# Performance work log

Hardware: AMD Instinct MI355X
Metric: run time of the kernel (lower is better)

## Reference

```python
import jax, jax.numpy as jnp
import numpy as np
from jax import lax

B, T, D_IN, D_PROJ, D_OUT, LORDER = 16, 2048, 1024, 512, 1024, 20


def setup_inputs() -> dict:
    key = jax.random.key(0)
    k1, k2, k3, k4 = jax.random.split(key, 4)
    s = 0.05
    return {
        "input": jax.random.normal(k1, (B, T, D_IN), dtype=jnp.float32),
        "in_cache": jnp.zeros((B, D_PROJ, LORDER - 1), dtype=jnp.float32),
        "W_lin": jax.random.normal(k2, (D_IN, D_PROJ), dtype=jnp.float32) * s,
        "conv_w": jax.random.normal(k3, (D_PROJ, LORDER), dtype=jnp.float32) * s,
        "W_aff": jax.random.normal(k4, (D_PROJ, D_OUT), dtype=jnp.float32) * s,
        "b_aff": jnp.zeros((D_OUT,), dtype=jnp.float32),
    }


def reference(input, in_cache, W_lin, conv_w, W_aff, b_aff):
    L = conv_w.shape[1]
    # 1) linear down-projection (no bias): [B,T,Din] -> [B,T,Dp]
    x = jnp.einsum("btd,dp->btp", input, W_lin)
    # 2) FSMN causal depthwise memory block with streaming cache
    xt = jnp.swapaxes(x, 1, 2)                       # [B,Dp,T]
    cat = jnp.concatenate([in_cache, xt], axis=2)    # [B,Dp,T+L-1]
    out_cache = cat[:, :, -(L - 1):]                 # last L-1 frames for next chunk
    # depthwise conv over time, VALID padding -> output length T
    y = lax.conv_general_dilated(
        cat, conv_w[:, None, :],                      # rhs [Dp,1,L]
        window_strides=(1,), padding="VALID",
        dimension_numbers=("NCH", "OIH", "NCH"),
        feature_group_count=conv_w.shape[0])
    m = jnp.swapaxes(y + xt, 1, 2)                   # residual add, back to [B,T,Dp]
    # 3) affine up-projection + 4) ReLU
    out = jax.nn.relu(jnp.einsum("btp,po->bto", m, W_aff) + b_aff)
    return (out, out_cache)
```

## Files before the change

### kernel.cpp

```cpp
#include <hip/hip_runtime.h>
#include <cstdint>
#include <cstddef>

#define B_  16
#define T_  2048
#define DIN 1024
#define DPJ 512
#define DOUT 1024
#define LORD 20
#define HALO (LORD - 1)
#define M_ROWS (B_ * T_)
#define OUT0_ELEMS ((size_t)M_ROWS * DOUT)
#define CACHE_ELEMS ((size_t)B_ * DPJ * (LORD - 1))

typedef __bf16 bf16_t;
typedef __bf16 bf16x2 __attribute__((ext_vector_type(2)));
typedef __bf16 bf16x4 __attribute__((ext_vector_type(4)));
typedef __bf16 bf16x8 __attribute__((ext_vector_type(8)));
typedef float  f32x4  __attribute__((ext_vector_type(4)));

__device__ __forceinline__ void async_load16(const bf16_t* g, bf16_t* lds_base) {
    __builtin_amdgcn_global_load_lds(
        (const __attribute__((address_space(1))) unsigned int*)g,
        (__attribute__((address_space(3))) unsigned int*)lds_base,
        16, 0, 0);
}

__global__ __launch_bounds__(256) void prep_weights(
    const float* __restrict__ Wl, const float* __restrict__ Wa,
    bf16_t* __restrict__ WlT, bf16_t* __restrict__ WaT) {
    int idx = blockIdx.x * 256 + threadIdx.x;
    const int n1 = DIN * DPJ;
    if (idx < n1) {
        int k = idx / DPJ, n = idx - k * DPJ;
        WlT[(size_t)n * DIN + k] = (bf16_t)Wl[idx];
    } else {
        int j = idx - n1;
        if (j < DPJ * DOUT) {
            int k = j / DOUT, n = j - k * DOUT;
            WaT[(size_t)n * DPJ + k] = (bf16_t)Wa[j];
        }
    }
}

__global__ __launch_bounds__(256) void gemm_f32a(
    const float* __restrict__ A, const bf16_t* __restrict__ Bt,
    bf16_t* __restrict__ C, const int M, const int N, const int K) {
    __shared__ bf16_t sA[128 * 64];
    __shared__ bf16_t sB[128 * 64];

    const int tid  = threadIdx.x;
    const int lane = tid & 63;
    const int wave = tid >> 6;
    const int row0 = blockIdx.x * 128;
    const int col0 = blockIdx.y * 128;

    const int lr   = lane >> 3;
    const int jsw  = (lane & 7) ^ lr;
    const bf16_t* gB0 = Bt + (size_t)(col0 + wave * 32 + lr) * K + jsw * 8;
    bf16_t* lB0 = sB + wave * 2048;

    const int ar  = tid >> 4;
    const int ac4 = tid & 15;
    const float* gA0 = A + (size_t)(row0 + ar) * K + ac4 * 4;
    const int aj = ac4 >> 1, ah = ac4 & 1;
    const int asw = ((aj ^ (ar & 7)) << 3) + ah * 4;

    const int wm = (wave >> 1) * 64;
    const int wn = (wave & 1) * 64;
    const int fr = lane & 15;
    const int fk = lane >> 4;

    const f32x4 zero = {0.f, 0.f, 0.f, 0.f};
    f32x4 acc[4][4];
#pragma unroll
    for (int mt = 0; mt < 4; ++mt)
#pragma unroll
        for (int nt = 0; nt < 4; ++nt) acc[mt][nt] = zero;

    for (int k0 = 0; k0 < K; k0 += 64) {
        __syncthreads();
        float4 av[8];
#pragma unroll
        for (int i = 0; i < 8; ++i)
            av[i] = *(const float4*)(gA0 + (size_t)i * 16 * K + k0);
#pragma unroll
        for (int c = 0; c < 4; ++c)
            async_load16(gB0 + (size_t)c * 8 * K + k0, lB0 + c * 512);
#pragma unroll
        for (int i = 0; i < 8; ++i) {
            bf16x4 o = { (bf16_t)av[i].x, (bf16_t)av[i].y,
                         (bf16_t)av[i].z, (bf16_t)av[i].w };
            *(bf16x4*)(sA + (i * 16 + ar) * 64 + asw) = o;
        }
        __syncthreads();

#pragma unroll
        for (int h = 0; h < 2; ++h) {
            bf16x8 af[4], bfr[4];
#pragma unroll
            for (int mt = 0; mt < 4; ++mt) {
                int r = wm + mt * 16 + fr;
                int j = h * 4 + fk;
                af[mt] = *(const bf16x8*)(sA + r * 64 + ((j ^ (r & 7)) << 3));
            }
#pragma unroll
            for (int nt = 0; nt < 4; ++nt) {
                int r = wn + nt * 16 + fr;
                int j = h * 4 + fk;
                bfr[nt] = *(const bf16x8*)(sB + r * 64 + ((j ^ (r & 7)) << 3));
            }
#pragma unroll
            for (int mt = 0; mt < 4; ++mt)
#pragma unroll
                for (int nt = 0; nt < 4; ++nt)
                    acc[mt][nt] = __builtin_amdgcn_mfma_f32_16x16x32_bf16(
                        af[mt], bfr[nt], acc[mt][nt], 0, 0, 0);
        }
    }

    const int er = row0 + wm + (lane >> 4) * 4;
    const int ec = col0 + wn + (lane & 15);
#pragma unroll
    for (int mt = 0; mt < 4; ++mt)
#pragma unroll
        for (int nt = 0; nt < 4; ++nt)
#pragma unroll
            for (int rr = 0; rr < 4; ++rr)
                C[(size_t)(er + mt * 16 + rr) * N + (ec + nt * 16)] =
                    (bf16_t)acc[mt][nt][rr];
}

__global__ __launch_bounds__(256) void gemm_bt_relu(
    const bf16_t* __restrict__ A, const bf16_t* __restrict__ Bt,
    float* __restrict__ C, const float* __restrict__ bias,
    const int M, const int N, const int K) {
    __shared__ bf16_t sA[128 * 64];
    __shared__ bf16_t sB[128 * 64];

    const int tid  = threadIdx.x;
    const int lane = tid & 63;
    const int wave = tid >> 6;
    const int row0 = blockIdx.x * 128;
    const int col0 = blockIdx.y * 128;

    const int lr   = lane >> 3;
    const int jsw  = (lane & 7) ^ lr;
    const bf16_t* gA0 = A  + (size_t)(row0 + wave * 32 + lr) * K + jsw * 8;
    const bf16_t* gB0 = Bt + (size_t)(col0 + wave * 32 + lr) * K + jsw * 8;
    bf16_t* lA0 = sA + wave * 2048;
    bf16_t* lB0 = sB + wave * 2048;

    const int wm = (wave >> 1) * 64;
    const int wn = (wave & 1) * 64;
    const int fr = lane & 15;
    const int fk = lane >> 4;

    const f32x4 zero = {0.f, 0.f, 0.f, 0.f};
    f32x4 acc[4][4];
#pragma unroll
    for (int mt = 0; mt < 4; ++mt)
#pragma unroll
        for (int nt = 0; nt < 4; ++nt) acc[mt][nt] = zero;

    for (int k0 = 0; k0 < K; k0 += 64) {
        __syncthreads();
#pragma unroll
        for (int c = 0; c < 4; ++c) {
            async_load16(gA0 + (size_t)c * 8 * K + k0, lA0 + c * 512);
            async_load16(gB0 + (size_t)c * 8 * K + k0, lB0 + c * 512);
        }
        __syncthreads();

#pragma unroll
        for (int h = 0; h < 2; ++h) {
            bf16x8 af[4], bfr[4];
#pragma unroll
            for (int mt = 0; mt < 4; ++mt) {
                int r = wm + mt * 16 + fr;
                int j = h * 4 + fk;
                af[mt] = *(const bf16x8*)(sA + r * 64 + ((j ^ (r & 7)) << 3));
            }
#pragma unroll
            for (int nt = 0; nt < 4; ++nt) {
                int r = wn + nt * 16 + fr;
                int j = h * 4 + fk;
                bfr[nt] = *(const bf16x8*)(sB + r * 64 + ((j ^ (r & 7)) << 3));
            }
#pragma unroll
            for (int mt = 0; mt < 4; ++mt)
#pragma unroll
                for (int nt = 0; nt < 4; ++nt)
                    acc[mt][nt] = __builtin_amdgcn_mfma_f32_16x16x32_bf16(
                        af[mt], bfr[nt], acc[mt][nt], 0, 0, 0);
        }
    }

    const int er = row0 + wm + (lane >> 4) * 4;
    const int ec = col0 + wn + (lane & 15);
#pragma unroll
    for (int nt = 0; nt < 4; ++nt) {
        float bb = bias[ec + nt * 16];
#pragma unroll
        for (int mt = 0; mt < 4; ++mt)
#pragma unroll
            for (int rr = 0; rr < 4; ++rr) {
                float v = acc[mt][nt][rr] + bb;
                C[(size_t)(er + mt * 16 + rr) * N + (ec + nt * 16)] =
                    v > 0.f ? v : 0.f;
            }
    }
}

#define TT 64
#define PPT 128
__global__ __launch_bounds__(256) void dwconv_tiled(
    const bf16_t* __restrict__ x, const float* __restrict__ cache,
    const float* __restrict__ cw, bf16_t* __restrict__ m) {
    __shared__ float sx[(TT + HALO) * PPT];

    const int tid = threadIdx.x;
    const int t0  = blockIdx.x * TT;
    const int b   = blockIdx.y;
    const int p0  = blockIdx.z * PPT;

    for (int c = tid; c < (TT + HALO) * PPT / 8; c += 256) {
        int r    = c >> 4;
        int col  = (c & 15) << 3;
        int trow = t0 - HALO + r;
        float* dst = sx + r * PPT + col;
        if (trow >= 0) {
            bf16x8 v = *(const bf16x8*)(x + ((size_t)(b * T_ + trow)) * DPJ + p0 + col);
#pragma unroll
            for (int i = 0; i < 8; ++i) dst[i] = (float)v[i];
        } else {
#pragma unroll
            for (int i = 0; i < 8; ++i)
                dst[i] = cache[((size_t)b * DPJ + p0 + col + i) * HALO + (trow + HALO)];
        }
    }
    __syncthreads();

    const int pp   = tid & 63;
    const int half = tid >> 6;
    const int tb   = half * 16;
    const float2* sx2 = (const float2*)sx;

    const int pg = p0 + 2 * pp;
    float2 w[LORD];
#pragma unroll
    for (int l = 0; l < LORD; ++l) {
        w[l].x = cw[pg * LORD + l];
        w[l].y = cw[(pg + 1) * LORD + l];
    }

    float2 win[LORD];
#pragma unroll
    for (int i = 0; i < HALO; ++i) win[i] = sx2[(tb + i) * 64 + pp];

#pragma unroll
    for (int tl = 0; tl < 16; ++tl) {
        float2 nv = sx2[(tb + tl + HALO) * 64 + pp];
        win[(tl + HALO) % LORD] = nv;
        float2 s = nv;
#pragma unroll
        for (int l = 0; l < LORD; ++l) {
            float2 v = win[(tl + l) % LORD];
            s.x += w[l].x * v.x;
            s.y += w[l].y * v.y;
        }
        bf16x2 o = { (bf16_t)s.x, (bf16_t)s.y };
        *(bf16x2*)(m + ((size_t)(b * T_ + t0 + tb + tl)) * DPJ + pg) = o;
    }
}

__global__ __launch_bounds__(256) void cache_out(
    const bf16_t* __restrict__ x, float* __restrict__ oc) {
    int idx = blockIdx.x * 256 + threadIdx.x;
    if (idx < (int)CACHE_ELEMS) {
        int b = idx / (DPJ * (LORD - 1));
        int rem = idx % (DPJ * (LORD - 1));
        int p = rem / (LORD - 1);
        int j = rem % (LORD - 1);
        oc[idx] = (float)x[((size_t)(b * T_ + T_ - (LORD - 1) + j)) * DPJ + p];
    }
}

extern "C" void kernel_launch(void* const* d_in, const int* in_sizes, int n_in,
                              void* d_out, int out_size, void* d_ws, size_t ws_size,
                              hipStream_t stream) {
    const float* input    = (const float*)d_in[0];
    const float* in_cache = (const float*)d_in[1];
    const float* W_lin    = (const float*)d_in[2];
    const float* conv_w   = (const float*)d_in[3];
    const float* W_aff    = (const float*)d_in[4];
    const float* b_aff    = (const float*)d_in[5];
    float* out = (float*)d_out;

    char* ws = (char*)d_ws;
    bf16_t* x_buf = (bf16_t*)(ws);
    bf16_t* m_buf = (bf16_t*)(ws + 33554432);
    bf16_t* WlinT = (bf16_t*)(ws + 67108864);
    bf16_t* WaffT = (bf16_t*)(ws + 67108864 + 1048576);

    prep_weights<<<(DIN * DPJ + DPJ * DOUT + 255) / 256, 256, 0, stream>>>(
        W_lin, W_aff, WlinT, WaffT);

    gemm_f32a<<<dim3(M_ROWS / 128, DPJ / 128), 256, 0, stream>>>(
        input, WlinT, x_buf, M_ROWS, DPJ, DIN);

    dwconv_tiled<<<dim3(T_ / TT, B_, DPJ / PPT), 256, 0, stream>>>(
        x_buf, in_cache, conv_w, m_buf);
    cache_out<<<(int)((CACHE_ELEMS + 255) / 256), 256, 0, stream>>>(
        x_buf, out + OUT0_ELEMS);

    gemm_bt_relu<<<dim3(M_ROWS / 128, DOUT / 128), 256, 0, stream>>>(
        m_buf, WaffT, out, b_aff, M_ROWS, DOUT, DPJ);
}
```

Baseline: 406.2 us.

## Async-load fp32 A tiles to LDS, swap grid order, fuse cache_out into dwconv

```diff
diff --git a/kernel.cpp b/kernel.cpp
--- a/kernel.cpp
+++ b/kernel.cpp
@@ -19,7 +19,7 @@
 typedef __bf16 bf16x8 __attribute__((ext_vector_type(8)));
 typedef float  f32x4  __attribute__((ext_vector_type(4)));
 
-__device__ __forceinline__ void async_load16(const bf16_t* g, bf16_t* lds_base) {
+__device__ __forceinline__ void async_load16(const void* g, void* lds_base) {
     __builtin_amdgcn_global_load_lds(
         (const __attribute__((address_space(1))) unsigned int*)g,
         (__attribute__((address_space(3))) unsigned int*)lds_base,
@@ -43,28 +43,35 @@
     }
 }
 
-__global__ __launch_bounds__(256) void gemm_f32a(
+__global__ __launch_bounds__(256) void gemm1_fused(
     const float* __restrict__ A, const bf16_t* __restrict__ Bt,
     bf16_t* __restrict__ C, const int M, const int N, const int K) {
-    __shared__ bf16_t sA[128 * 64];
-    __shared__ bf16_t sB[128 * 64];
+    __shared__ float  sAf[128 * 64];
+    __shared__ bf16_t sB [128 * 64];
 
     const int tid  = threadIdx.x;
     const int lane = tid & 63;
     const int wave = tid >> 6;
-    const int row0 = blockIdx.x * 128;
-    const int col0 = blockIdx.y * 128;
-
-    const int lr   = lane >> 3;
-    const int jsw  = (lane & 7) ^ lr;
+    const int col0 = blockIdx.x * 128;
+    const int row0 = blockIdx.y * 128;
+
+    const int hi = lane >> 4;
+    const int lo = lane & 15;
+    size_t aoff[8];
+#pragma unroll
+    for (int c = 0; c < 8; ++c) {
+        int rloc  = wave * 32 + c * 4 + hi;
+        int chunk = lo ^ (((c & 3) << 2) | hi);
+        aoff[c] = (size_t)(row0 + rloc) * K + chunk * 4;
+    }
+    float* lA[8];
+#pragma unroll
+    for (int c = 0; c < 8; ++c) lA[c] = sAf + (wave * 32 + c * 4) * 64;
+
+    const int lr  = lane >> 3;
+    const int jsw = (lane & 7) ^ lr;
     const bf16_t* gB0 = Bt + (size_t)(col0 + wave * 32 + lr) * K + jsw * 8;
     bf16_t* lB0 = sB + wave * 2048;
-
-    const int ar  = tid >> 4;
-    const int ac4 = tid & 15;
-    const float* gA0 = A + (size_t)(row0 + ar) * K + ac4 * 4;
-    const int aj = ac4 >> 1, ah = ac4 & 1;
-    const int asw = ((aj ^ (ar & 7)) << 3) + ah * 4;
 
     const int wm = (wave >> 1) * 64;
     const int wn = (wave & 1) * 64;
@@ -80,19 +87,11 @@
 
     for (int k0 = 0; k0 < K; k0 += 64) {
         __syncthreads();
-        float4 av[8];
-#pragma unroll
-        for (int i = 0; i < 8; ++i)
-            av[i] = *(const float4*)(gA0 + (size_t)i * 16 * K + k0);
+#pragma unroll
+        for (int c = 0; c < 8; ++c) async_load16(A + aoff[c] + k0, lA[c]);
 #pragma unroll
         for (int c = 0; c < 4; ++c)
             async_load16(gB0 + (size_t)c * 8 * K + k0, lB0 + c * 512);
-#pragma unroll
-        for (int i = 0; i < 8; ++i) {
-            bf16x4 o = { (bf16_t)av[i].x, (bf16_t)av[i].y,
-                         (bf16_t)av[i].z, (bf16_t)av[i].w };
-            *(bf16x4*)(sA + (i * 16 + ar) * 64 + asw) = o;
-        }
         __syncthreads();
 
 #pragma unroll
@@ -100,9 +99,13 @@
             bf16x8 af[4], bfr[4];
 #pragma unroll
             for (int mt = 0; mt < 4; ++mt) {
-                int r = wm + mt * 16 + fr;
-                int j = h * 4 + fk;
-                af[mt] = *(const bf16x8*)(sA + r * 64 + ((j ^ (r & 7)) << 3));
+                int r  = wm + mt * 16 + fr;
+                int c0 = h * 8 + fk * 2;
+                f32x4 a0 = *(const f32x4*)(sAf + r * 64 + ((c0 ^ fr) << 2));
+                f32x4 a1 = *(const f32x4*)(sAf + r * 64 + (((c0 + 1) ^ fr) << 2));
+                bf16x8 v = { (bf16_t)a0[0], (bf16_t)a0[1], (bf16_t)a0[2], (bf16_t)a0[3],
+                             (bf16_t)a1[0], (bf16_t)a1[1], (bf16_t)a1[2], (bf16_t)a1[3] };
+                af[mt] = v;
             }
 #pragma unroll
             for (int nt = 0; nt < 4; ++nt) {
@@ -141,8 +144,8 @@
     const int tid  = threadIdx.x;
     const int lane = tid & 63;
     const int wave = tid >> 6;
-    const int row0 = blockIdx.x * 128;
-    const int col0 = blockIdx.y * 128;
+    const int col0 = blockIdx.x * 128;
+    const int row0 = blockIdx.y * 128;
 
     const int lr   = lane >> 3;
     const int jsw  = (lane & 7) ^ lr;
@@ -216,7 +219,8 @@
 #define PPT 128
 __global__ __launch_bounds__(256) void dwconv_tiled(
     const bf16_t* __restrict__ x, const float* __restrict__ cache,
-    const float* __restrict__ cw, bf16_t* __restrict__ m) {
+    const float* __restrict__ cw, bf16_t* __restrict__ m,
+    float* __restrict__ oc) {
     __shared__ float sx[(TT + HALO) * PPT];
 
     const int tid = threadIdx.x;
@@ -272,17 +276,13 @@
         bf16x2 o = { (bf16_t)s.x, (bf16_t)s.y };
         *(bf16x2*)(m + ((size_t)(b * T_ + t0 + tb + tl)) * DPJ + pg) = o;
     }
-}
-
-__global__ __launch_bounds__(256) void cache_out(
-    const bf16_t* __restrict__ x, float* __restrict__ oc) {
-    int idx = blockIdx.x * 256 + threadIdx.x;
-    if (idx < (int)CACHE_ELEMS) {
-        int b = idx / (DPJ * (LORD - 1));
-        int rem = idx % (DPJ * (LORD - 1));
-        int p = rem / (LORD - 1);
-        int j = rem % (LORD - 1);
-        oc[idx] = (float)x[((size_t)(b * T_ + T_ - (LORD - 1) + j)) * DPJ + p];
+
+    if (blockIdx.x == (T_ / TT) - 1) {
+        for (int i = tid; i < PPT * HALO; i += 256) {
+            int pl = i / HALO;
+            int j  = i - pl * HALO;
+            oc[((size_t)b * DPJ + p0 + pl) * HALO + j] = sx[(64 + j) * PPT + pl];
+        }
     }
 }
 
@@ -306,14 +306,12 @@
     prep_weights<<<(DIN * DPJ + DPJ * DOUT + 255) / 256, 256, 0, stream>>>(
         W_lin, W_aff, WlinT, WaffT);
 
-    gemm_f32a<<<dim3(M_ROWS / 128, DPJ / 128), 256, 0, stream>>>(
+    gemm1_fused<<<dim3(DPJ / 128, M_ROWS / 128), 256, 0, stream>>>(
         input, WlinT, x_buf, M_ROWS, DPJ, DIN);
 
     dwconv_tiled<<<dim3(T_ / TT, B_, DPJ / PPT), 256, 0, stream>>>(
-        x_buf, in_cache, conv_w, m_buf);
-    cache_out<<<(int)((CACHE_ELEMS + 255) / 256), 256, 0, stream>>>(
-        x_buf, out + OUT0_ELEMS);
-
-    gemm_bt_relu<<<dim3(M_ROWS / 128, DOUT / 128), 256, 0, stream>>>(
+        x_buf, in_cache, conv_w, m_buf, out + OUT0_ELEMS);
+
+    gemm_bt_relu<<<dim3(DOUT / 128, M_ROWS / 128), 256, 0, stream>>>(
         m_buf, WaffT, out, b_aff, M_ROWS, DOUT, DPJ);
 }
```

Measured after the change: 371.8 us. -8.5%, faster.
